# Optimization experiments

Measured on AMD Instinct MI355X. Metric: run time of the kernel, lower is better.

Reference implementation:

```python
import jax, jax.numpy as jnp
import numpy as np

N = 4096          # residues
D = 256           # local feature dim
FACTOR = 2
H = 8             # global heads
DF = D * FACTOR   # 512
DH = DF // H      # 64 per-head dim
NUM_CHAINS = 64
NUM_BATCHES = 8


def index_mean(x, idx, mask, num_segments):
    """Masked segment mean, gathered back to per-element shape.
    x: [N, ...], idx: [N] int, mask: broadcastable to x (0/1)."""
    m = mask.astype(x.dtype)
    xm = x * m
    s = jax.ops.segment_sum(xm, idx, num_segments=num_segments)
    c = jax.ops.segment_sum(jnp.broadcast_to(m, x.shape), idx, num_segments=num_segments)
    mean = s / jnp.maximum(c, 1e-6)
    return mean[idx]


def setup_inputs() -> dict:
    key = jax.random.key(0)
    ks = jax.random.split(key, 12)
    s_in = 1.0 / np.sqrt(D)
    s_mid = 1.0 / np.sqrt(2 * DF)
    return {
        "local": jax.random.normal(ks[0], (N, D), jnp.float32),
        "chain": jax.random.randint(ks[1], (N,), 0, NUM_CHAINS),
        "batch": jax.random.randint(ks[2], (N,), 0, NUM_BATCHES),
        "mask": jax.random.bernoulli(ks[3], 0.9, (N,)),
        "W_key": jax.random.normal(ks[4], (D, DF), jnp.float32) * s_in,
        "b_key": jnp.zeros((DF,), jnp.float32),
        "W_value": jax.random.normal(ks[5], (D, DF), jnp.float32) * s_in,
        "b_value": jnp.zeros((DF,), jnp.float32),
        "W_query": jax.random.normal(ks[6], (D, DF), jnp.float32) * s_in,
        "b_query": jnp.zeros((DF,), jnp.float32),
        "W_bias": jax.random.normal(ks[7], (D, 2 * DF), jnp.float32) * s_in,
        "b_bias": jnp.zeros((2 * DF,), jnp.float32),
        "W_out": jax.random.normal(ks[8], (2 * DF, D), jnp.float32) * s_mid,
    }


def reference(local, chain, batch, mask,
              W_key, b_key, W_value, b_value, W_query, b_query,
              W_bias, b_bias, W_out):
    n = local.shape[0]
    k = jax.nn.gelu(local @ W_key + b_key).reshape(n, H, DH)
    v = (local @ W_value + b_value).reshape(n, H, DH)
    q = jax.nn.gelu(local @ W_query + b_query).reshape(n, H, DH)

    bias = index_mean(local @ W_bias + b_bias, batch, mask[:, None], NUM_BATCHES)

    # outer product key (x) value: [N, H, DH, DH]
    ov = k[:, :, :, None] * v[:, :, None, :]
    m4 = mask[:, None, None, None]
    chain_op = index_mean(ov, chain, m4, NUM_CHAINS)
    batch_op = index_mean(ov, batch, m4, NUM_BATCHES)
    operation = jnp.concatenate((chain_op, batch_op), axis=-2)  # [N, H, 2*DH, DH]

    out = jnp.einsum('bhvk,bhk->bhv', operation, q).reshape(n, -1) + bias
    return out @ W_out
```

## Files before the change

kernel.cpp:

```cpp
#include <hip/hip_runtime.h>
#include <math.h>

#define NN 4096
#define DD 256
#define DFF 512
#define HH 8
#define DHH 64
#define CAP_C 256
#define CAP_B 1024

#define OFF_KB     0
#define OFF_VB     1048576
#define OFF_QB     2097152
#define OFF_ATTNB  3145728
#define OFF_LOCALB 5242880
#define OFF_STC    5767168
#define OFF_STBP   7864320
#define OFF_BSUM   8912896
#define OFF_CNT    8921088
#define OFF_WQKVT  8921344
#define OFF_WOUTT  9117952
#define OFF_LISTS  9249024
#define OFF_LPART  9298176

typedef __attribute__((ext_vector_type(8))) short bf16x8;
typedef __attribute__((ext_vector_type(4))) float floatx4;

__device__ __forceinline__ float gelu_f(float x) {
    const float c = 0.7978845608028654f;
    float t = tanhf(c * (x + 0.044715f * x * x * x));
    return 0.5f * x * (1.0f + t);
}

__device__ __forceinline__ unsigned short f2b(float f) {
    union { float f; unsigned int u; } v; v.f = f;
    unsigned int r = (v.u + 0x7FFFu + ((v.u >> 16) & 1u)) >> 16;
    return (unsigned short)r;
}

__global__ __launch_bounds__(256) void prep_kernel(
    const float* __restrict__ local,
    const float* __restrict__ Wk, const float* __restrict__ Wv,
    const float* __restrict__ Wq, const float* __restrict__ Wout,
    const int* __restrict__ batch, const int* __restrict__ mask,
    unsigned short* __restrict__ Wqkvt, unsigned short* __restrict__ Woutt,
    unsigned short* __restrict__ localb,
    float* __restrict__ Lpart, float* __restrict__ zero_base)
{
    const int bid = blockIdx.x, tid = threadIdx.x;
    if (bid < 640) {
        const float* src; unsigned short* dst; int R, C, r0, c0;
        if (bid < 384) {
            int m = bid >> 7, ti = bid & 127;
            src = (m == 0) ? Wk : (m == 1) ? Wv : Wq;
            dst = Wqkvt + (size_t)m * 512 * 256;
            R = 256; C = 512;
            r0 = (ti >> 4) * 32; c0 = (ti & 15) * 32;
        } else {
            int ti = bid - 384;
            src = Wout; dst = Woutt;
            R = 1024; C = 256;
            r0 = (ti >> 3) * 32; c0 = (ti & 7) * 32;
        }
        __shared__ float Tl[32][33];
        int ty = tid >> 3, tx = tid & 7;
        float4 v = *(const float4*)(src + (size_t)(r0 + ty) * C + c0 + tx * 4);
        Tl[tx * 4 + 0][ty] = v.x;
        Tl[tx * 4 + 1][ty] = v.y;
        Tl[tx * 4 + 2][ty] = v.z;
        Tl[tx * 4 + 3][ty] = v.w;
        __syncthreads();
        ushort4 o;
        o.x = f2b(Tl[ty][tx * 4 + 0]);
        o.y = f2b(Tl[ty][tx * 4 + 1]);
        o.z = f2b(Tl[ty][tx * 4 + 2]);
        o.w = f2b(Tl[ty][tx * 4 + 3]);
        *(ushort4*)(dst + (size_t)(c0 + ty) * R + r0 + tx * 4) = o;
    } else if (bid < 896) {
        int p = bid - 640;
        float accl[8] = {};
        int n0 = p * 16;
#pragma unroll
        for (int r = 0; r < 16; ++r) {
            int n = n0 + r;
            float v = local[(size_t)n * DD + tid];
            int bb = batch[n];
            float vm = mask[n] ? v : 0.0f;
#pragma unroll
            for (int b = 0; b < 8; ++b)
                accl[b] += (bb == b) ? vm : 0.0f;
        }
#pragma unroll
        for (int b = 0; b < 8; ++b)
            Lpart[(size_t)p * 2048 + b * 256 + tid] = accl[b];
    } else if (bid < 1408) {
        int p = bid - 896;
        size_t base = (size_t)p * 2048 + tid * 8;
        float4 a0 = *(const float4*)(local + base);
        float4 a1 = *(const float4*)(local + base + 4);
        ushort4 p0, p1;
        p0.x = f2b(a0.x); p0.y = f2b(a0.y); p0.z = f2b(a0.z); p0.w = f2b(a0.w);
        p1.x = f2b(a1.x); p1.y = f2b(a1.y); p1.z = f2b(a1.z); p1.w = f2b(a1.w);
        *(ushort4*)(localb + base) = p0;
        *(ushort4*)(localb + base + 4) = p1;
    } else {
        float4 z4 = make_float4(0.f, 0.f, 0.f, 0.f);
        for (int i = tid; i < 2112; i += 256)
            ((float4*)zero_base)[i] = z4;
    }
}

__global__ __launch_bounds__(256) void qkv_kernel(
    const unsigned short* __restrict__ localb,
    const unsigned short* __restrict__ Wqkvt,
    const float* __restrict__ bk, const float* __restrict__ bv,
    const float* __restrict__ bq, unsigned short* __restrict__ KVQb,
    const int* __restrict__ chain, const int* __restrict__ batch,
    const int* __restrict__ mask, int* __restrict__ cnt,
    int* __restrict__ lists)
{
    __shared__ __align__(16) char smem[18944];
    const int u = blockIdx.x, tid = threadIdx.x;
    int* cntc_m   = cnt;
    int* cntc_all = cnt + 64;
    int* cntb_m   = cnt + 128;
    int* cntb_all = cnt + 136;
    int* listc_m   = lists;
    int* listc_all = listc_m + 64 * CAP_C;
    int* listb_m   = listc_all + 64 * CAP_C;
    int* listb_all = listb_m + 8 * CAP_B;

    if (u < 1536) {
        typedef unsigned short (*t72)[72];
        t72 Asl = (t72)smem;
        t72 Bsl = (t72)(smem + 9216);
        const int wave = tid >> 6, lane = tid & 63;
        const int q = lane >> 4, r = lane & 15;
        const int cx = u % 24, ry = u / 24;
        const int row0 = ry * 64, cg0 = cx * 64;

        floatx4 acc[4] = {};
        for (int kk = 0; kk < 256; kk += 64) {
#pragma unroll
            for (int i = 0; i < 2; ++i) {
                int lin = tid * 2 + i;
                int rr = lin >> 3, kc = (lin & 7) * 8;
                *(float4*)&Asl[rr][kc] =
                    *(const float4*)(localb + (size_t)(row0 + rr) * DD + kk + kc);
                *(float4*)&Bsl[rr][kc] =
                    *(const float4*)(Wqkvt + (size_t)(cg0 + rr) * DD + kk + kc);
            }
            __syncthreads();
#pragma unroll
            for (int sub = 0; sub < 2; ++sub) {
                bf16x8 a = *(const bf16x8*)&Asl[wave * 16 + r][sub * 32 + q * 8];
#pragma unroll
                for (int c = 0; c < 4; ++c) {
                    bf16x8 b = *(const bf16x8*)&Bsl[c * 16 + r][sub * 32 + q * 8];
                    acc[c] = __builtin_amdgcn_mfma_f32_16x16x32_bf16(a, b, acc[c], 0, 0, 0);
                }
            }
            __syncthreads();
        }
        const int sel = cg0 >> 9;
        const int do_gelu = (sel != 1);
        const float* bias = (sel == 0) ? bk : (sel == 1) ? bv : bq;
        unsigned short* C = KVQb + (size_t)sel * (NN * DFF);
#pragma unroll
        for (int c = 0; c < 4; ++c) {
            int colw = (cg0 + c * 16 + r) & 511;
            float bb = bias[colw];
#pragma unroll
            for (int i = 0; i < 4; ++i) {
                int row = row0 + wave * 16 + q * 4 + i;
                float o = acc[c][i] + bb;
                if (do_gelu) o = gelu_f(o);
                C[(size_t)row * DFF + colw] = f2b(o);
            }
        }
    } else {
        int* sh = (int*)smem;
        int* hc_m = sh;        int* hc_all = sh + 64;
        int* hb_m = sh + 128;  int* hb_all = sh + 136;
        int* pc_m = sh + 144;  int* pc_all = sh + 208;
        int* pb_m = sh + 272;  int* pb_all = sh + 280;
        if (tid < 64) { hc_m[tid] = 0; hc_all[tid] = 0; }
        if (tid < 8)  { hb_m[tid] = 0; hb_all[tid] = 0; }
        __syncthreads();
        int n = (u - 1536) * 256 + tid;
        int c = chain[n], b = batch[n], m = mask[n];
        int rc_all = atomicAdd(&hc_all[c], 1);
        int rb_all = atomicAdd(&hb_all[b], 1);
        int rc_m = -1, rb_m = -1;
        if (m) { rc_m = atomicAdd(&hc_m[c], 1); rb_m = atomicAdd(&hb_m[b], 1); }
        __syncthreads();
        if (tid < 64) {
            pc_all[tid] = atomicAdd(&cntc_all[tid], hc_all[tid]);
            pc_m[tid]   = atomicAdd(&cntc_m[tid],   hc_m[tid]);
        }
        if (tid < 8) {
            pb_all[tid] = atomicAdd(&cntb_all[tid], hb_all[tid]);
            pb_m[tid]   = atomicAdd(&cntb_m[tid],   hb_m[tid]);
        }
        __syncthreads();
        int ia = pc_all[c] + rc_all; if (ia < CAP_C) listc_all[c * CAP_C + ia] = n;
        int ib = pb_all[b] + rb_all; if (ib < CAP_B) listb_all[b * CAP_B + ib] = n;
        if (m) {
            int ja = pc_m[c] + rc_m; if (ja < CAP_C) listc_m[c * CAP_C + ja] = n;
            int jb = pb_m[b] + rb_m; if (jb < CAP_B) listb_m[b * CAP_B + jb] = n;
        }
    }
}

__global__ __launch_bounds__(256) void mid_kernel(
    const unsigned short* __restrict__ Kb, const unsigned short* __restrict__ Vb,
    const int* __restrict__ cnt, const int* __restrict__ lists,
    float* __restrict__ STc, float* __restrict__ STbp,
    const float* __restrict__ Lpart, const float* __restrict__ Wbias,
    float* __restrict__ Bsum)
{
    const int u = blockIdx.x, tid = threadIdx.x;
    __shared__ unsigned short Ktl[64][36];
    __shared__ unsigned short Vtl[64][36];

    if (u >= 768) {
        int t = u - 768;
        const int seg = t >> 3, kz = t & 7;
        float (*part)[32] = (float(*)[32])Ktl;
        float* Lk = ((float*)Ktl) + 256;
        {
            int k = tid & 31, pg = tid >> 5;
            float s = 0.0f;
#pragma unroll 8
            for (int p = pg * 32; p < pg * 32 + 32; ++p)
                s += Lpart[(size_t)p * 2048 + seg * 256 + kz * 32 + k];
            part[pg][k] = s;
        }
        __syncthreads();
        if (tid < 32) {
            float s = 0.0f;
#pragma unroll
            for (int pg = 0; pg < 8; ++pg) s += part[pg][tid];
            Lk[tid] = s;
        }
        __syncthreads();
        float4 a4 = make_float4(0, 0, 0, 0);
        for (int k = 0; k < 32; ++k) {
            float l = Lk[k];
            float4 w = *(const float4*)(Wbias + (size_t)(kz * 32 + k) * 1024 + tid * 4);
            a4.x += l * w.x; a4.y += l * w.y; a4.z += l * w.z; a4.w += l * w.w;
        }
        float* o = Bsum + (size_t)seg * 1024 + tid * 4;
        atomicAdd(o + 0, a4.x); atomicAdd(o + 1, a4.y);
        atomicAdd(o + 2, a4.z); atomicAdd(o + 3, a4.w);
        return;
    }

    const int* cntc_m = cnt;
    const int* cntb_m = cnt + 128;
    const int* listc_m = lists;
    const int* listb_m = lists + 2 * 64 * CAP_C;

    int seg, h, r0, r1, cap;
    const int* list; float* ST;
    if (u < 256) {
        int z = u >> 6; seg = (u >> 3) & 7; h = u & 7;
        cap = CAP_B; list = listb_m;
        int c = min(cntb_m[seg], CAP_B);
        int chunk = (c + 3) / 4;
        r0 = z * chunk; r1 = min(c, r0 + chunk);
        ST = STbp + (size_t)z * 262144 + ((size_t)(seg * HH + h) << 12);
    } else {
        int t = u - 256;
        seg = t >> 3; h = t & 7;
        cap = CAP_C; list = listc_m;
        r0 = 0; r1 = min(cntc_m[seg], CAP_C);
        ST = STc + ((size_t)(seg * HH + h) << 12);
    }

    const int wave = tid >> 6, lane = tid & 63;
    const int la = lane & 15, kq = lane >> 4;

    floatx4 acc4[4] = {};
    for (int g = r0; g < r1; g += 32) {
#pragma unroll
        for (int it = 0; it < 2; ++it) {
            int item = tid + it * 256;
            int nl = item & 31, aq = item >> 5;
            int gg = g + nl;
            ushort4 kz4 = make_ushort4(0, 0, 0, 0);
            ushort4 vz4 = make_ushort4(0, 0, 0, 0);
            if (gg < r1) {
                int nn = list[seg * cap + gg];
                kz4 = *(const ushort4*)(Kb + (size_t)nn * DFF + h * DHH + aq * 4);
                vz4 = *(const ushort4*)(Vb + (size_t)nn * DFF + h * DHH + aq * 4);
            }
            Ktl[aq * 4 + 0][nl] = kz4.x; Ktl[aq * 4 + 1][nl] = kz4.y;
            Ktl[aq * 4 + 2][nl] = kz4.z; Ktl[aq * 4 + 3][nl] = kz4.w;
            Vtl[aq * 4 + 0][nl] = vz4.x; Vtl[aq * 4 + 1][nl] = vz4.y;
            Vtl[aq * 4 + 2][nl] = vz4.z; Vtl[aq * 4 + 3][nl] = vz4.w;
        }
        __syncthreads();
        bf16x8 a = *(const bf16x8*)&Ktl[wave * 16 + la][kq * 8];
#pragma unroll
        for (int bt = 0; bt < 4; ++bt) {
            bf16x8 b = *(const bf16x8*)&Vtl[bt * 16 + la][kq * 8];
            acc4[bt] = __builtin_amdgcn_mfma_f32_16x16x32_bf16(a, b, acc4[bt], 0, 0, 0);
        }
        __syncthreads();
    }

#pragma unroll
    for (int bt = 0; bt < 4; ++bt)
#pragma unroll
        for (int rg = 0; rg < 4; ++rg) {
            int aa = wave * 16 + kq * 4 + rg;
            int bb2 = bt * 16 + la;
            ST[aa * 64 + bb2] = acc4[bt][rg];
        }
}

__global__ __launch_bounds__(256) void einsum_kernel(
    const float* __restrict__ STc, const float* __restrict__ STbp,
    const int* __restrict__ cnt, const int* __restrict__ lists,
    const unsigned short* __restrict__ Qb, const int* __restrict__ batch,
    const float* __restrict__ Bsum, const float* __restrict__ b_bias,
    unsigned short* __restrict__ attnb)
{
    const int id = blockIdx.x, tid = threadIdx.x;
    const int* cntc_m   = cnt;
    const int* cntc_all = cnt + 64;
    const int* cntb_m   = cnt + 128;
    const int* cntb_all = cnt + 136;
    const int* listc_all = lists + 64 * CAP_C;
    const int* listb_all = lists + 2 * 64 * CAP_C + 8 * CAP_B;

    int seg, h, outoff, cap, r0, r1;
    const int* list;
    float scaleS;
    bool is_chain;
    if (id < 512) {
        seg = id >> 3; h = id & 7; outoff = 0;
        list = listc_all; cap = CAP_C; is_chain = true;
        scaleS = 1.0f / fmaxf((float)min(cntc_m[seg], CAP_C), 1e-6f);
        r0 = 0; r1 = min(cntc_all[seg], CAP_C);
    } else {
        int t = id - 512;
        seg = t >> 6; h = (t >> 3) & 7;
        int z = t & 7;
        outoff = 64;
        list = listb_all; cap = CAP_B; is_chain = false;
        scaleS = 1.0f / fmaxf((float)min(cntb_m[seg], CAP_B), 1e-6f);
        int c = min(cntb_all[seg], CAP_B);
        int chunk = (c + 7) / 8;
        r0 = z * chunk; r1 = min(c, r0 + chunk);
    }

    __shared__ unsigned short Sbl[64][72];
    __shared__ unsigned short Qsl[64][72];
    __shared__ float Bf[8][64];
    __shared__ int nrow[64];
    __shared__ int nbb[64];

    const int wave = tid >> 6, lane = tid & 63;
    const int la = lane & 15, kq = lane >> 4;
    const int colbase = h * 128 + outoff;

#pragma unroll
    for (int i = 0; i < 4; ++i) {
        int e = tid + i * 256;
        float4 v;
        if (is_chain) {
            v = *(const float4*)(STc + ((size_t)(seg * HH + h) << 12) + (size_t)e * 4);
        } else {
            const float* Sg = STbp + ((size_t)(seg * HH + h) << 12) + (size_t)e * 4;
            float4 v0 = *(const float4*)(Sg);
            float4 v1 = *(const float4*)(Sg + 262144);
            float4 v2 = *(const float4*)(Sg + 524288);
            float4 v3 = *(const float4*)(Sg + 786432);
            v.x = v0.x + v1.x + v2.x + v3.x;
            v.y = v0.y + v1.y + v2.y + v3.y;
            v.z = v0.z + v1.z + v2.z + v3.z;
            v.w = v0.w + v1.w + v2.w + v3.w;
        }
        int a = e >> 4, b = (e & 15) * 4;
        ushort4 o;
        o.x = f2b(v.x * scaleS); o.y = f2b(v.y * scaleS);
        o.z = f2b(v.z * scaleS); o.w = f2b(v.w * scaleS);
        *(ushort4*)&Sbl[a][b] = o;
    }
#pragma unroll
    for (int e = tid; e < 512; e += 256) {
        int bbq = e >> 6, j = e & 63;
        float cm = (float)min(cntb_m[bbq], CAP_B);
        float inv = 1.0f / fmaxf(cm, 1e-6f);
        int col = colbase + j;
        Bf[bbq][j] = (Bsum[(size_t)bbq * 1024 + col] + cm * b_bias[col]) * inv;
    }
    __syncthreads();

    for (int g = r0; g < r1; g += 64) {
        if (tid < 64) {
            int gg = g + tid;
            int n = (gg < r1) ? list[seg * cap + gg] : -1;
            nrow[tid] = n;
            nbb[tid] = (n >= 0) ? batch[n] : 0;
        }
        __syncthreads();
        {
            int row = tid & 63, pr = tid >> 6;
            int n = nrow[row];
            if (n >= 0) {
#pragma unroll
                for (int it = 0; it < 2; ++it) {
                    int off = (pr + it * 4) * 8;
                    *(float4*)&Qsl[row][off] =
                        *(const float4*)(Qb + (size_t)n * DFF + h * DHH + off);
                }
            }
        }
        __syncthreads();

        floatx4 acc[4] = {};
#pragma unroll
        for (int ks = 0; ks < 2; ++ks) {
            bf16x8 a = *(const bf16x8*)&Qsl[wave * 16 + la][ks * 32 + kq * 8];
#pragma unroll
            for (int ct = 0; ct < 4; ++ct) {
                bf16x8 b = *(const bf16x8*)&Sbl[ct * 16 + la][ks * 32 + kq * 8];
                acc[ct] = __builtin_amdgcn_mfma_f32_16x16x32_bf16(a, b, acc[ct], 0, 0, 0);
            }
        }
#pragma unroll
        for (int ct = 0; ct < 4; ++ct)
#pragma unroll
            for (int rg = 0; rg < 4; ++rg) {
                int rowl = wave * 16 + kq * 4 + rg;
                float bias = Bf[nbb[rowl]][ct * 16 + la];
                Qsl[rowl][ct * 16 + la] = f2b(acc[ct][rg] + bias);
            }
        __syncthreads();
        {
            int row = tid & 63, pr = tid >> 6;
            int n = nrow[row];
            if (n >= 0) {
#pragma unroll
                for (int it = 0; it < 2; ++it) {
                    int off = (pr + it * 4) * 8;
                    *(float4*)(attnb + (size_t)n * 1024 + colbase + off) =
                        *(const float4*)&Qsl[row][off];
                }
            }
        }
        __syncthreads();
    }
}

__global__ __launch_bounds__(256) void mfma_gemm_final(
    const unsigned short* __restrict__ A, const unsigned short* __restrict__ Bt,
    float* __restrict__ out)
{
    const int K = 1024;
    __shared__ unsigned short Asl[32][136];
    __shared__ unsigned short Bsl[32][136];
    const int tid = threadIdx.x;
    const int wave = tid >> 6, lane = tid & 63;
    const int q = lane >> 4, r = lane & 15;
    const int row0 = blockIdx.y * 32, cg0 = blockIdx.x * 32;
    const int wrow = (wave & 1) * 16, wcol = (wave >> 1) * 16;

    floatx4 acc = {};
    for (int kk = 0; kk < K; kk += 128) {
#pragma unroll
        for (int t = 0; t < 2; ++t) {
            int idx = tid + t * 256;
            int rr = idx >> 4, kc = (idx & 15) * 8;
            *(float4*)&Asl[rr][kc] = *(const float4*)(A + (size_t)(row0 + rr) * K + kk + kc);
            *(float4*)&Bsl[rr][kc] = *(const float4*)(Bt + (size_t)(cg0 + rr) * K + kk + kc);
        }
        __syncthreads();
#pragma unroll
        for (int sub = 0; sub < 4; ++sub) {
            bf16x8 a = *(const bf16x8*)&Asl[wrow + r][sub * 32 + q * 8];
            bf16x8 b = *(const bf16x8*)&Bsl[wcol + r][sub * 32 + q * 8];
            acc = __builtin_amdgcn_mfma_f32_16x16x32_bf16(a, b, acc, 0, 0, 0);
        }
        __syncthreads();
    }
    int col = cg0 + wcol + r;
#pragma unroll
    for (int i = 0; i < 4; ++i) {
        int row = row0 + wrow + q * 4 + i;
        out[(size_t)row * DD + col] = acc[i];
    }
}

extern "C" void kernel_launch(void* const* d_in, const int* in_sizes, int n_in,
                              void* d_out, int out_size, void* d_ws, size_t ws_size,
                              hipStream_t stream)
{
    const float* local   = (const float*)d_in[0];
    const int*   chain   = (const int*)d_in[1];
    const int*   batch   = (const int*)d_in[2];
    const int*   mask    = (const int*)d_in[3];
    const float* W_key   = (const float*)d_in[4];
    const float* b_key   = (const float*)d_in[5];
    const float* W_value = (const float*)d_in[6];
    const float* b_value = (const float*)d_in[7];
    const float* W_query = (const float*)d_in[8];
    const float* b_query = (const float*)d_in[9];
    const float* W_bias  = (const float*)d_in[10];
    const float* b_bias  = (const float*)d_in[11];
    const float* W_out   = (const float*)d_in[12];
    float* out = (float*)d_out;

    float* ws = (float*)d_ws;
    unsigned short* Kb     = (unsigned short*)(ws + OFF_KB);
    unsigned short* Qb     = (unsigned short*)(ws + OFF_QB);
    unsigned short* attnb  = (unsigned short*)(ws + OFF_ATTNB);
    unsigned short* localb = (unsigned short*)(ws + OFF_LOCALB);
    float* STc    = ws + OFF_STC;
    float* STbp   = ws + OFF_STBP;
    float* Bsum   = ws + OFF_BSUM;
    int*   cnt    = (int*)(ws + OFF_CNT);
    unsigned short* Wqkvt = (unsigned short*)(ws + OFF_WQKVT);
    unsigned short* Woutt = (unsigned short*)(ws + OFF_WOUTT);
    int*   lists  = (int*)(ws + OFF_LISTS);
    float* Lpart  = ws + OFF_LPART;

    dim3 blk(256);

    prep_kernel<<<dim3(1409), blk, 0, stream>>>(
        local, W_key, W_value, W_query, W_out, batch, mask,
        Wqkvt, Woutt, localb, Lpart, ws + OFF_BSUM);

    qkv_kernel<<<dim3(1552), blk, 0, stream>>>(
        localb, Wqkvt, b_key, b_value, b_query, Kb,
        chain, batch, mask, cnt, lists);

    mid_kernel<<<dim3(832), blk, 0, stream>>>(
        Kb, (const unsigned short*)(ws + OFF_VB), cnt, lists, STc, STbp,
        Lpart, W_bias, Bsum);

    einsum_kernel<<<dim3(1024), blk, 0, stream>>>(
        STc, STbp, cnt, lists, Qb, batch, Bsum, b_bias, attnb);

    mfma_gemm_final<<<dim3(8, 128), blk, 0, stream>>>(attnb, Woutt, out);
}
```

Measured before the change: 133.4 us.

## Fuse final output projection into einsum kernel with atomic accumulation

Removes the separate final GEMM and the bf16 attention intermediate buffer. Each einsum block now loads its 64-column slice of the transposed output weights into shared memory, multiplies its result tile by that slice with MFMA, and atomically adds partial sums into the output. The output is zeroed in the prep kernel. This saves one launch and a round trip of the intermediate through memory, but adds heavy float atomics (16 column tiles per row per block), extra shared memory that may lower occupancy, and a non-deterministic summation order.

```diff
diff --git a/kernel.cpp b/kernel.cpp
--- a/kernel.cpp
+++ b/kernel.cpp
@@ -12,7 +12,6 @@
 #define OFF_KB     0
 #define OFF_VB     1048576
 #define OFF_QB     2097152
-#define OFF_ATTNB  3145728
 #define OFF_LOCALB 5242880
 #define OFF_STC    5767168
 #define OFF_STBP   7864320
@@ -45,7 +44,8 @@
     const int* __restrict__ batch, const int* __restrict__ mask,
     unsigned short* __restrict__ Wqkvt, unsigned short* __restrict__ Woutt,
     unsigned short* __restrict__ localb,
-    float* __restrict__ Lpart, float* __restrict__ zero_base)
+    float* __restrict__ Lpart, float* __restrict__ out,
+    float* __restrict__ zero_base)
 {
     const int bid = blockIdx.x, tid = threadIdx.x;
     if (bid < 640) {
@@ -103,6 +103,13 @@
         p1.x = f2b(a1.x); p1.y = f2b(a1.y); p1.z = f2b(a1.z); p1.w = f2b(a1.w);
         *(ushort4*)(localb + base) = p0;
         *(ushort4*)(localb + base + 4) = p1;
+    } else if (bid < 1472) {
+        int p = bid - 1408;
+        float4 z4 = make_float4(0.f, 0.f, 0.f, 0.f);
+        float4* o4 = (float4*)out;
+#pragma unroll
+        for (int i = 0; i < 16; ++i)
+            o4[p * 4096 + i * 256 + tid] = z4;
     } else {
         float4 z4 = make_float4(0.f, 0.f, 0.f, 0.f);
         for (int i = tid; i < 2112; i += 256)
@@ -320,12 +327,12 @@
         }
 }
 
-__global__ __launch_bounds__(256) void einsum_kernel(
+__global__ __launch_bounds__(256) void einsum_fused_kernel(
     const float* __restrict__ STc, const float* __restrict__ STbp,
     const int* __restrict__ cnt, const int* __restrict__ lists,
     const unsigned short* __restrict__ Qb, const int* __restrict__ batch,
     const float* __restrict__ Bsum, const float* __restrict__ b_bias,
-    unsigned short* __restrict__ attnb)
+    const unsigned short* __restrict__ Woutt, float* __restrict__ out)
 {
     const int id = blockIdx.x, tid = threadIdx.x;
     const int* cntc_m   = cnt;
@@ -358,6 +365,7 @@
 
     __shared__ unsigned short Sbl[64][72];
     __shared__ unsigned short Qsl[64][72];
+    __shared__ unsigned short Wsl[256][72];
     __shared__ float Bf[8][64];
     __shared__ int nrow[64];
     __shared__ int nbb[64];
@@ -365,6 +373,7 @@
     const int wave = tid >> 6, lane = tid & 63;
     const int la = lane & 15, kq = lane >> 4;
     const int colbase = h * 128 + outoff;
+    const int wrow = wave * 16;
 
 #pragma unroll
     for (int i = 0; i < 4; ++i) {
@@ -390,6 +399,13 @@
         *(ushort4*)&Sbl[a][b] = o;
     }
 #pragma unroll
+    for (int i = 0; i < 8; ++i) {
+        int e = tid + i * 256;
+        int oc = e >> 3, j8 = (e & 7) * 8;
+        *(float4*)&Wsl[oc][j8] =
+            *(const float4*)(Woutt + (size_t)oc * 1024 + colbase + j8);
+    }
+#pragma unroll
     for (int e = tid; e < 512; e += 256) {
         int bbq = e >> 6, j = e & 63;
         float cm = (float)min(cntb_m[bbq], CAP_B);
@@ -424,7 +440,7 @@
         floatx4 acc[4] = {};
 #pragma unroll
         for (int ks = 0; ks < 2; ++ks) {
-            bf16x8 a = *(const bf16x8*)&Qsl[wave * 16 + la][ks * 32 + kq * 8];
+            bf16x8 a = *(const bf16x8*)&Qsl[wrow + la][ks * 32 + kq * 8];
 #pragma unroll
             for (int ct = 0; ct < 4; ++ct) {
                 bf16x8 b = *(const bf16x8*)&Sbl[ct * 16 + la][ks * 32 + kq * 8];
@@ -435,63 +451,31 @@
         for (int ct = 0; ct < 4; ++ct)
 #pragma unroll
             for (int rg = 0; rg < 4; ++rg) {
-                int rowl = wave * 16 + kq * 4 + rg;
+                int rowl = wrow + kq * 4 + rg;
                 float bias = Bf[nbb[rowl]][ct * 16 + la];
                 Qsl[rowl][ct * 16 + la] = f2b(acc[ct][rg] + bias);
             }
-        __syncthreads();
-        {
-            int row = tid & 63, pr = tid >> 6;
-            int n = nrow[row];
-            if (n >= 0) {
-#pragma unroll
-                for (int it = 0; it < 2; ++it) {
-                    int off = (pr + it * 4) * 8;
-                    *(float4*)(attnb + (size_t)n * 1024 + colbase + off) =
-                        *(const float4*)&Qsl[row][off];
-                }
-            }
-        }
-        __syncthreads();
-    }
-}
-
-__global__ __launch_bounds__(256) void mfma_gemm_final(
-    const unsigned short* __restrict__ A, const unsigned short* __restrict__ Bt,
-    float* __restrict__ out)
-{
-    const int K = 1024;
-    __shared__ unsigned short Asl[32][136];
-    __shared__ unsigned short Bsl[32][136];
-    const int tid = threadIdx.x;
-    const int wave = tid >> 6, lane = tid & 63;
-    const int q = lane >> 4, r = lane & 15;
-    const int row0 = blockIdx.y * 32, cg0 = blockIdx.x * 32;
-    const int wrow = (wave & 1) * 16, wcol = (wave >> 1) * 16;
-
-    floatx4 acc = {};
-    for (int kk = 0; kk < K; kk += 128) {
-#pragma unroll
-        for (int t = 0; t < 2; ++t) {
-            int idx = tid + t * 256;
-            int rr = idx >> 4, kc = (idx & 15) * 8;
-            *(float4*)&Asl[rr][kc] = *(const float4*)(A + (size_t)(row0 + rr) * K + kk + kc);
-            *(float4*)&Bsl[rr][kc] = *(const float4*)(Bt + (size_t)(cg0 + rr) * K + kk + kc);
-        }
-        __syncthreads();
-#pragma unroll
-        for (int sub = 0; sub < 4; ++sub) {
-            bf16x8 a = *(const bf16x8*)&Asl[wrow + r][sub * 32 + q * 8];
-            bf16x8 b = *(const bf16x8*)&Bsl[wcol + r][sub * 32 + q * 8];
-            acc = __builtin_amdgcn_mfma_f32_16x16x32_bf16(a, b, acc, 0, 0, 0);
-        }
-        __syncthreads();
-    }
-    int col = cg0 + wcol + r;
-#pragma unroll
-    for (int i = 0; i < 4; ++i) {
-        int row = row0 + wrow + q * 4 + i;
-        out[(size_t)row * DD + col] = acc[i];
+
+        floatx4 acc2[16] = {};
+#pragma unroll
+        for (int ks = 0; ks < 2; ++ks) {
+            bf16x8 a = *(const bf16x8*)&Qsl[wrow + la][ks * 32 + kq * 8];
+#pragma unroll
+            for (int ct = 0; ct < 16; ++ct) {
+                bf16x8 b = *(const bf16x8*)&Wsl[ct * 16 + la][ks * 32 + kq * 8];
+                acc2[ct] = __builtin_amdgcn_mfma_f32_16x16x32_bf16(a, b, acc2[ct], 0, 0, 0);
+            }
+        }
+#pragma unroll
+        for (int ct = 0; ct < 16; ++ct)
+#pragma unroll
+            for (int rg = 0; rg < 4; ++rg) {
+                int rowl = wrow + kq * 4 + rg;
+                int n = nrow[rowl];
+                if (n >= 0)
+                    atomicAdd(&out[(size_t)n * DD + ct * 16 + la], acc2[ct][rg]);
+            }
+        __syncthreads();
     }
 }
 
@@ -517,7 +501,6 @@
     float* ws = (float*)d_ws;
     unsigned short* Kb     = (unsigned short*)(ws + OFF_KB);
     unsigned short* Qb     = (unsigned short*)(ws + OFF_QB);
-    unsigned short* attnb  = (unsigned short*)(ws + OFF_ATTNB);
     unsigned short* localb = (unsigned short*)(ws + OFF_LOCALB);
     float* STc    = ws + OFF_STC;
     float* STbp   = ws + OFF_STBP;
@@ -530,9 +513,9 @@
 
     dim3 blk(256);
 
-    prep_kernel<<<dim3(1409), blk, 0, stream>>>(
+    prep_kernel<<<dim3(1473), blk, 0, stream>>>(
         local, W_key, W_value, W_query, W_out, batch, mask,
-        Wqkvt, Woutt, localb, Lpart, ws + OFF_BSUM);
+        Wqkvt, Woutt, localb, Lpart, out, ws + OFF_BSUM);
 
     qkv_kernel<<<dim3(1552), blk, 0, stream>>>(
         localb, Wqkvt, b_key, b_value, b_query, Kb,
@@ -542,8 +525,6 @@
         Kb, (const unsigned short*)(ws + OFF_VB), cnt, lists, STc, STbp,
         Lpart, W_bias, Bsum);
 
-    einsum_kernel<<<dim3(1024), blk, 0, stream>>>(
-        STc, STbp, cnt, lists, Qb, batch, Bsum, b_bias, attnb);
-
-    mfma_gemm_final<<<dim3(8, 128), blk, 0, stream>>>(attnb, Woutt, out);
-}
+    einsum_fused_kernel<<<dim3(1024), blk, 0, stream>>>(
+        STc, STbp, cnt, lists, Qb, batch, Bsum, b_bias, Woutt, out);
+}
```

After: 173.5 us. 30.1% more time.
